# Kernel optimization log

Measured on AMD Instinct MI355X. Metric: run time of the kernel, lower is better.

The kernel has to match this reference:

```python
import jax, jax.numpy as jnp
import numpy as np

LOG2PI = float(np.log(2.0 * np.pi))
B, D = 8192, 4096


def setup_inputs() -> dict:
    key = jax.random.key(0)
    k1, k2, k3, k4, k5 = jax.random.split(key, 5)
    return {
        "z": jax.random.normal(k1, (B, D), dtype=jnp.float32),
        "mean": jax.random.normal(k2, (B, D), dtype=jnp.float32),
        "log_sd": jax.random.normal(k3, (B, D), dtype=jnp.float32),
        "target": jax.random.randint(k4, (B,), 0, 2, dtype=jnp.int64 if jax.config.jax_enable_x64 else jnp.int32),
        "logdet": jax.random.normal(k5, (B,), dtype=jnp.float32),
    }


def reference(z, mean, log_sd, target, logdet):
    # Per-class (binary) masked statistics, exactly matching the torch forward:
    #   mu_cls = mean[target==j].mean(0); log_sd_cls likewise;
    #   log_p  = gaussian_log_p(z_cls, mu_cls, log_sd_cls).sum(feature).mean(batch)
    def per_class(j):
        m = (target == j).astype(z.dtype)          # (B,)
        cnt = m.sum()
        ld_mean = (logdet * m).sum() / cnt          # scalar
        mu = (mean * m[:, None]).sum(0) / cnt       # (D,)
        lsd = (log_sd * m[:, None]).sum(0) / cnt    # (D,)
        # gaussian log-prob summed over features, per sample -> (B,)
        lp = (-0.5 * LOG2PI - lsd
              - 0.5 * (z - mu) ** 2 * jnp.exp(-2.0 * lsd)).sum(1)
        lp_mean = (lp * m).sum() / cnt              # masked mean over class members
        return ld_mean, mu, lsd, lp_mean

    res = [per_class(j) for j in (0, 1)]
    logdet_total = jnp.stack([r[0] for r in res])   # (2,)
    mus_per_class = jnp.stack([r[1] for r in res])  # (2, D)
    log_sds_per_class = jnp.stack([r[2] for r in res])  # (2, D)
    log_p_total = jnp.stack([r[3] for r in res])    # (2,)
    prior_logprob = (log_p_total + logdet_total).mean()
    return prior_logprob, mus_per_class, log_sds_per_class, log_p_total
```

## Files before the change

kernel.cpp:

```cpp
#include <hip/hip_runtime.h>

#define B_SZ 8192
#define D_SZ 4096
#define PC   128
#define RP   (B_SZ / PC)


__device__ __forceinline__ void acc4(float4& a, const float4 v) {
    a.x += v.x; a.y += v.y; a.z += v.z; a.w += v.w;
}
__device__ __forceinline__ void fma4(float4& a, const float4 v, const float k) {
    a.x = fmaf(v.x, k, a.x); a.y = fmaf(v.y, k, a.y);
    a.z = fmaf(v.z, k, a.z); a.w = fmaf(v.w, k, a.w);
}
__device__ __forceinline__ float4 sq4(const float4 v) {
    return {v.x * v.x, v.y * v.y, v.z * v.z, v.w * v.w};
}

__global__ __launch_bounds__(256, 4)
void colsum_kernel(const float* __restrict__ z,
                   const float* __restrict__ mean,
                   const float* __restrict__ lsd,
                   const int* __restrict__ target,
                   float* __restrict__ part) {
    const int col = blockIdx.x * 1024 + (threadIdx.x << 2);
    const int r   = blockIdx.y;
    const size_t base0 = (size_t)(r * RP) * D_SZ + col;

    const float* pz = z    + base0;
    const float* pm = mean + base0;
    const float* pl = lsd  + base0;
    const int*   pt = target + r * RP;

    float4 mA = {0,0,0,0}, m1 = {0,0,0,0};
    float4 lA = {0,0,0,0}, l1 = {0,0,0,0};
    float4 zA = {0,0,0,0}, z1 = {0,0,0,0};
    float4 qA = {0,0,0,0}, q1 = {0,0,0,0};

    for (int it = 0; it < RP / 4; ++it) {
        const float4 vz0 = *(const float4*)(pz);
        const float4 vz1 = *(const float4*)(pz + 1 * D_SZ);
        const float4 vz2 = *(const float4*)(pz + 2 * D_SZ);
        const float4 vz3 = *(const float4*)(pz + 3 * D_SZ);
        const float4 vm0 = *(const float4*)(pm);
        const float4 vm1 = *(const float4*)(pm + 1 * D_SZ);
        const float4 vm2 = *(const float4*)(pm + 2 * D_SZ);
        const float4 vm3 = *(const float4*)(pm + 3 * D_SZ);
        const float4 vl0 = *(const float4*)(pl);
        const float4 vl1 = *(const float4*)(pl + 1 * D_SZ);
        const float4 vl2 = *(const float4*)(pl + 2 * D_SZ);
        const float4 vl3 = *(const float4*)(pl + 3 * D_SZ);
        const int4   t   = *(const int4*)(pt);
        __builtin_amdgcn_sched_barrier(0);

        const float k0 = (t.x == 1) ? 1.f : 0.f;
        const float k1 = (t.y == 1) ? 1.f : 0.f;
        const float k2 = (t.z == 1) ? 1.f : 0.f;
        const float k3 = (t.w == 1) ? 1.f : 0.f;

        acc4(mA, vm0); fma4(m1, vm0, k0);
        acc4(mA, vm1); fma4(m1, vm1, k1);
        acc4(mA, vm2); fma4(m1, vm2, k2);
        acc4(mA, vm3); fma4(m1, vm3, k3);

        acc4(lA, vl0); fma4(l1, vl0, k0);
        acc4(lA, vl1); fma4(l1, vl1, k1);
        acc4(lA, vl2); fma4(l1, vl2, k2);
        acc4(lA, vl3); fma4(l1, vl3, k3);

        acc4(zA, vz0); fma4(z1, vz0, k0);
        acc4(zA, vz1); fma4(z1, vz1, k1);
        acc4(zA, vz2); fma4(z1, vz2, k2);
        acc4(zA, vz3); fma4(z1, vz3, k3);

        const float4 q0 = sq4(vz0); acc4(qA, q0); fma4(q1, q0, k0);
        const float4 qq1 = sq4(vz1); acc4(qA, qq1); fma4(q1, qq1, k1);
        const float4 q2 = sq4(vz2); acc4(qA, q2); fma4(q1, q2, k2);
        const float4 q3 = sq4(vz3); acc4(qA, q3); fma4(q1, q3, k3);

        pz += 4 * D_SZ; pm += 4 * D_SZ; pl += 4 * D_SZ; pt += 4;
    }

    *(float4*)(part + ((size_t)(0 * PC + r)) * D_SZ + col) = mA;
    *(float4*)(part + ((size_t)(1 * PC + r)) * D_SZ + col) = m1;
    *(float4*)(part + ((size_t)(2 * PC + r)) * D_SZ + col) = lA;
    *(float4*)(part + ((size_t)(3 * PC + r)) * D_SZ + col) = l1;
    *(float4*)(part + ((size_t)(4 * PC + r)) * D_SZ + col) = zA;
    *(float4*)(part + ((size_t)(5 * PC + r)) * D_SZ + col) = z1;
    *(float4*)(part + ((size_t)(6 * PC + r)) * D_SZ + col) = qA;
    *(float4*)(part + ((size_t)(7 * PC + r)) * D_SZ + col) = q1;
}

__global__ __launch_bounds__(256)
void reduce_count_kernel(const float* __restrict__ part,
                         const int* __restrict__ target,
                         const float* __restrict__ logdet,
                         float* __restrict__ red,
                         float* __restrict__ sc) {
    if (blockIdx.x == 64) {
        __shared__ float rsm[3][4];
        float c = 0.f, a = 0.f, o = 0.f;
#pragma unroll
        for (int k = 0; k < 8; ++k) {
            const int i = k * 1024 + (threadIdx.x << 2);
            const int4   t = *(const int4*)(target + i);
            const float4 l = *(const float4*)(logdet + i);
            const float n0 = (t.x == 1) ? 1.f : 0.f;
            const float n1 = (t.y == 1) ? 1.f : 0.f;
            const float n2 = (t.z == 1) ? 1.f : 0.f;
            const float n3 = (t.w == 1) ? 1.f : 0.f;
            c += n0 + n1 + n2 + n3;
            a += l.x + l.y + l.z + l.w;
            o += l.x * n0 + l.y * n1 + l.z * n2 + l.w * n3;
        }
        for (int off = 32; off > 0; off >>= 1) {
            c += __shfl_down(c, off);
            a += __shfl_down(a, off);
            o += __shfl_down(o, off);
        }
        const int w = threadIdx.x >> 6;
        if ((threadIdx.x & 63) == 0) { rsm[0][w] = c; rsm[1][w] = a; rsm[2][w] = o; }
        __syncthreads();
        if (threadIdx.x == 0) {
            sc[0] = rsm[0][0] + rsm[0][1] + rsm[0][2] + rsm[0][3];
            sc[1] = rsm[1][0] + rsm[1][1] + rsm[1][2] + rsm[1][3];
            sc[2] = rsm[2][0] + rsm[2][1] + rsm[2][2] + rsm[2][3];
        }
        return;
    }
    const int seg = blockIdx.x >> 3;
    const int sub = blockIdx.x & 7;
    const int col = (sub >> 1) * 1024 + (threadIdx.x << 2);
    const int r0  = (sub & 1) * (PC / 2);
    float4 acc = {0,0,0,0};
    for (int r = r0; r < r0 + PC / 2; ++r) {
        const float4 v = *(const float4*)(part + ((size_t)seg * PC + r) * D_SZ + col);
        acc4(acc, v);
    }
    *(float4*)(red + ((size_t)((sub & 1) * 8 + seg)) * D_SZ + col) = acc;
}

__global__ __launch_bounds__(256)
void finalize_cols_kernel(const float* __restrict__ red,
                          const float* __restrict__ sc,
                          double* __restrict__ dslots,
                          float* __restrict__ out) {
    const int d = blockIdx.x * 256 + threadIdx.x;
    const float cnt1 = sc[0];
    const float cnt0 = (float)B_SZ - cnt1;

#define RSEG(s) (red[(s) * D_SZ + d] + red[(8 + (s)) * D_SZ + d])
    const float ma = RSEG(0), m1 = RSEG(1);
    const float la = RSEG(2), l1 = RSEG(3);
    const float za = RSEG(4), z1 = RSEG(5);
    const float qa = RSEG(6), q1 = RSEG(7);
#undef RSEG

    const float mu1 = m1 / cnt1, mu0 = (ma - m1) / cnt0;
    const float ls1 = l1 / cnt1, ls0 = (la - l1) / cnt0;

    out[1 + d]            = mu0;
    out[1 + D_SZ + d]     = mu1;
    out[1 + 2 * D_SZ + d] = ls0;
    out[1 + 3 * D_SZ + d] = ls1;

    const float z0 = za - z1, q0 = qa - q1;
    const double w0 = 0.5 * exp(-2.0 * (double)ls0);
    const double w1 = 0.5 * exp(-2.0 * (double)ls1);
    double S0 = w0 * ((double)q0 - 2.0 * (double)mu0 * (double)z0 + (double)cnt0 * (double)mu0 * (double)mu0);
    double S1 = w1 * ((double)q1 - 2.0 * (double)mu1 * (double)z1 + (double)cnt1 * (double)mu1 * (double)mu1);
    double L0 = (double)ls0;
    double L1 = (double)ls1;

    for (int off = 32; off > 0; off >>= 1) {
        S0 += __shfl_down(S0, off);
        S1 += __shfl_down(S1, off);
        L0 += __shfl_down(L0, off);
        L1 += __shfl_down(L1, off);
    }
    if ((threadIdx.x & 63) == 0) {
        double* wd = dslots + (blockIdx.x * 4 + (threadIdx.x >> 6)) * 4;
        wd[0] = S0; wd[1] = S1; wd[2] = L0; wd[3] = L1;
    }
}

__global__ void finalize_scalars_kernel(const float* __restrict__ sc,
                                        const double* __restrict__ dslots,
                                        float* __restrict__ out) {
    const double* p = dslots + threadIdx.x * 4;
    double S0 = p[0], S1 = p[1], L0 = p[2], L1 = p[3];
    for (int off = 32; off > 0; off >>= 1) {
        S0 += __shfl_down(S0, off);
        S1 += __shfl_down(S1, off);
        L0 += __shfl_down(L0, off);
        L1 += __shfl_down(L1, off);
    }
    if (threadIdx.x == 0) {
        const double LOG2PI = 1.8378770664093453;
        const double cnt1 = (double)sc[0];
        const double cnt0 = (double)B_SZ - cnt1;
        const double ldm1 = (double)sc[2] / cnt1;
        const double ldm0 = ((double)sc[1] - (double)sc[2]) / cnt0;

        const double c0 = -0.5 * LOG2PI * (double)D_SZ - L0;
        const double c1 = -0.5 * LOG2PI * (double)D_SZ - L1;
        const double lp0 = c0 - S0 / cnt0;
        const double lp1 = c1 - S1 / cnt1;

        out[1 + 4 * D_SZ + 0] = (float)lp0;
        out[1 + 4 * D_SZ + 1] = (float)lp1;
        out[0] = (float)(0.5 * ((lp0 + ldm0) + (lp1 + ldm1)));
    }
}

extern "C" void kernel_launch(void* const* d_in, const int* in_sizes, int n_in,
                              void* d_out, int out_size, void* d_ws, size_t ws_size,
                              hipStream_t stream) {
    const float* z      = (const float*)d_in[0];
    const float* mean   = (const float*)d_in[1];
    const float* log_sd = (const float*)d_in[2];
    const int*   target = (const int*)d_in[3];
    const float* logdet = (const float*)d_in[4];
    float* out = (float*)d_out;
    float* ws  = (float*)d_ws;

    float*  part   = ws;
    float*  red    = ws + (size_t)PC * 8 * D_SZ;
    float*  sc     = red + 16 * D_SZ;
    double* dslots = (double*)(sc + 8);

    colsum_kernel<<<dim3(D_SZ / 1024, PC), 256, 0, stream>>>(z, mean, log_sd, target, part);
    reduce_count_kernel<<<65, 256, 0, stream>>>(part, target, logdet, red, sc);
    finalize_cols_kernel<<<D_SZ / 256, 256, 0, stream>>>(red, sc, dslots, out);
    finalize_scalars_kernel<<<1, 64, 0, stream>>>(sc, dslots, out);
}
```

Baseline: 88.51 us.

## Double row partitions, fold count reduction into stage1, widen partial reduce

```diff
diff --git a/kernel.cpp b/kernel.cpp
--- a/kernel.cpp
+++ b/kernel.cpp
@@ -2,8 +2,6 @@
 
 #define B_SZ 8192
 #define D_SZ 4096
-#define PC   128
-#define RP   (B_SZ / PC)
 
 
 __device__ __forceinline__ void acc4(float4& a, const float4 v) {
@@ -17,87 +15,18 @@
     return {v.x * v.x, v.y * v.y, v.z * v.z, v.w * v.w};
 }
 
+template <int PC>
 __global__ __launch_bounds__(256, 4)
-void colsum_kernel(const float* __restrict__ z,
+void stage1_kernel(const float* __restrict__ z,
                    const float* __restrict__ mean,
                    const float* __restrict__ lsd,
                    const int* __restrict__ target,
-                   float* __restrict__ part) {
-    const int col = blockIdx.x * 1024 + (threadIdx.x << 2);
-    const int r   = blockIdx.y;
-    const size_t base0 = (size_t)(r * RP) * D_SZ + col;
-
-    const float* pz = z    + base0;
-    const float* pm = mean + base0;
-    const float* pl = lsd  + base0;
-    const int*   pt = target + r * RP;
-
-    float4 mA = {0,0,0,0}, m1 = {0,0,0,0};
-    float4 lA = {0,0,0,0}, l1 = {0,0,0,0};
-    float4 zA = {0,0,0,0}, z1 = {0,0,0,0};
-    float4 qA = {0,0,0,0}, q1 = {0,0,0,0};
-
-    for (int it = 0; it < RP / 4; ++it) {
-        const float4 vz0 = *(const float4*)(pz);
-        const float4 vz1 = *(const float4*)(pz + 1 * D_SZ);
-        const float4 vz2 = *(const float4*)(pz + 2 * D_SZ);
-        const float4 vz3 = *(const float4*)(pz + 3 * D_SZ);
-        const float4 vm0 = *(const float4*)(pm);
-        const float4 vm1 = *(const float4*)(pm + 1 * D_SZ);
-        const float4 vm2 = *(const float4*)(pm + 2 * D_SZ);
-        const float4 vm3 = *(const float4*)(pm + 3 * D_SZ);
-        const float4 vl0 = *(const float4*)(pl);
-        const float4 vl1 = *(const float4*)(pl + 1 * D_SZ);
-        const float4 vl2 = *(const float4*)(pl + 2 * D_SZ);
-        const float4 vl3 = *(const float4*)(pl + 3 * D_SZ);
-        const int4   t   = *(const int4*)(pt);
-        __builtin_amdgcn_sched_barrier(0);
-
-        const float k0 = (t.x == 1) ? 1.f : 0.f;
-        const float k1 = (t.y == 1) ? 1.f : 0.f;
-        const float k2 = (t.z == 1) ? 1.f : 0.f;
-        const float k3 = (t.w == 1) ? 1.f : 0.f;
-
-        acc4(mA, vm0); fma4(m1, vm0, k0);
-        acc4(mA, vm1); fma4(m1, vm1, k1);
-        acc4(mA, vm2); fma4(m1, vm2, k2);
-        acc4(mA, vm3); fma4(m1, vm3, k3);
-
-        acc4(lA, vl0); fma4(l1, vl0, k0);
-        acc4(lA, vl1); fma4(l1, vl1, k1);
-        acc4(lA, vl2); fma4(l1, vl2, k2);
-        acc4(lA, vl3); fma4(l1, vl3, k3);
-
-        acc4(zA, vz0); fma4(z1, vz0, k0);
-        acc4(zA, vz1); fma4(z1, vz1, k1);
-        acc4(zA, vz2); fma4(z1, vz2, k2);
-        acc4(zA, vz3); fma4(z1, vz3, k3);
-
-        const float4 q0 = sq4(vz0); acc4(qA, q0); fma4(q1, q0, k0);
-        const float4 qq1 = sq4(vz1); acc4(qA, qq1); fma4(q1, qq1, k1);
-        const float4 q2 = sq4(vz2); acc4(qA, q2); fma4(q1, q2, k2);
-        const float4 q3 = sq4(vz3); acc4(qA, q3); fma4(q1, q3, k3);
-
-        pz += 4 * D_SZ; pm += 4 * D_SZ; pl += 4 * D_SZ; pt += 4;
-    }
-
-    *(float4*)(part + ((size_t)(0 * PC + r)) * D_SZ + col) = mA;
-    *(float4*)(part + ((size_t)(1 * PC + r)) * D_SZ + col) = m1;
-    *(float4*)(part + ((size_t)(2 * PC + r)) * D_SZ + col) = lA;
-    *(float4*)(part + ((size_t)(3 * PC + r)) * D_SZ + col) = l1;
-    *(float4*)(part + ((size_t)(4 * PC + r)) * D_SZ + col) = zA;
-    *(float4*)(part + ((size_t)(5 * PC + r)) * D_SZ + col) = z1;
-    *(float4*)(part + ((size_t)(6 * PC + r)) * D_SZ + col) = qA;
-    *(float4*)(part + ((size_t)(7 * PC + r)) * D_SZ + col) = q1;
-}
-
-__global__ __launch_bounds__(256)
-void reduce_count_kernel(const float* __restrict__ part,
-                         const int* __restrict__ target,
-                         const float* __restrict__ logdet,
-                         float* __restrict__ red,
-                         float* __restrict__ sc) {
-    if (blockIdx.x == 64) {
+                   const float* __restrict__ logdet,
+                   float* __restrict__ part,
+                   float* __restrict__ sc) {
+    constexpr int RP = B_SZ / PC;
+
+    if (blockIdx.x == 4 * PC) {
         __shared__ float rsm[3][4];
         float c = 0.f, a = 0.f, o = 0.f;
 #pragma unroll
@@ -128,16 +57,89 @@
         }
         return;
     }
-    const int seg = blockIdx.x >> 3;
-    const int sub = blockIdx.x & 7;
-    const int col = (sub >> 1) * 1024 + (threadIdx.x << 2);
-    const int r0  = (sub & 1) * (PC / 2);
+
+    const int col = (blockIdx.x & 3) * 1024 + (threadIdx.x << 2);
+    const int r   = blockIdx.x >> 2;
+    const size_t base0 = (size_t)(r * RP) * D_SZ + col;
+
+    const float* pz = z    + base0;
+    const float* pm = mean + base0;
+    const float* pl = lsd  + base0;
+    const int*   pt = target + r * RP;
+
+    float4 mA = {0,0,0,0}, m1 = {0,0,0,0};
+    float4 lA = {0,0,0,0}, l1 = {0,0,0,0};
+    float4 zA = {0,0,0,0}, z1 = {0,0,0,0};
+    float4 qA = {0,0,0,0}, q1 = {0,0,0,0};
+
+    for (int it = 0; it < RP / 4; ++it) {
+        const float4 vz0 = *(const float4*)(pz);
+        const float4 vz1 = *(const float4*)(pz + 1 * D_SZ);
+        const float4 vz2 = *(const float4*)(pz + 2 * D_SZ);
+        const float4 vz3 = *(const float4*)(pz + 3 * D_SZ);
+        const float4 vm0 = *(const float4*)(pm);
+        const float4 vm1 = *(const float4*)(pm + 1 * D_SZ);
+        const float4 vm2 = *(const float4*)(pm + 2 * D_SZ);
+        const float4 vm3 = *(const float4*)(pm + 3 * D_SZ);
+        const float4 vl0 = *(const float4*)(pl);
+        const float4 vl1 = *(const float4*)(pl + 1 * D_SZ);
+        const float4 vl2 = *(const float4*)(pl + 2 * D_SZ);
+        const float4 vl3 = *(const float4*)(pl + 3 * D_SZ);
+        const int4   t   = *(const int4*)(pt);
+        __builtin_amdgcn_sched_barrier(0);
+
+        const float k0 = (t.x == 1) ? 1.f : 0.f;
+        const float k1 = (t.y == 1) ? 1.f : 0.f;
+        const float k2 = (t.z == 1) ? 1.f : 0.f;
+        const float k3 = (t.w == 1) ? 1.f : 0.f;
+
+        acc4(mA, vm0); fma4(m1, vm0, k0);
+        acc4(mA, vm1); fma4(m1, vm1, k1);
+        acc4(mA, vm2); fma4(m1, vm2, k2);
+        acc4(mA, vm3); fma4(m1, vm3, k3);
+
+        acc4(lA, vl0); fma4(l1, vl0, k0);
+        acc4(lA, vl1); fma4(l1, vl1, k1);
+        acc4(lA, vl2); fma4(l1, vl2, k2);
+        acc4(lA, vl3); fma4(l1, vl3, k3);
+
+        acc4(zA, vz0); fma4(z1, vz0, k0);
+        acc4(zA, vz1); fma4(z1, vz1, k1);
+        acc4(zA, vz2); fma4(z1, vz2, k2);
+        acc4(zA, vz3); fma4(z1, vz3, k3);
+
+        const float4 q0  = sq4(vz0); acc4(qA, q0);  fma4(q1, q0,  k0);
+        const float4 qq1 = sq4(vz1); acc4(qA, qq1); fma4(q1, qq1, k1);
+        const float4 q2  = sq4(vz2); acc4(qA, q2);  fma4(q1, q2,  k2);
+        const float4 q3  = sq4(vz3); acc4(qA, q3);  fma4(q1, q3,  k3);
+
+        pz += 4 * D_SZ; pm += 4 * D_SZ; pl += 4 * D_SZ; pt += 4;
+    }
+
+    *(float4*)(part + ((size_t)(0 * PC + r)) * D_SZ + col) = mA;
+    *(float4*)(part + ((size_t)(1 * PC + r)) * D_SZ + col) = m1;
+    *(float4*)(part + ((size_t)(2 * PC + r)) * D_SZ + col) = lA;
+    *(float4*)(part + ((size_t)(3 * PC + r)) * D_SZ + col) = l1;
+    *(float4*)(part + ((size_t)(4 * PC + r)) * D_SZ + col) = zA;
+    *(float4*)(part + ((size_t)(5 * PC + r)) * D_SZ + col) = z1;
+    *(float4*)(part + ((size_t)(6 * PC + r)) * D_SZ + col) = qA;
+    *(float4*)(part + ((size_t)(7 * PC + r)) * D_SZ + col) = q1;
+}
+
+__global__ __launch_bounds__(256)
+void reduce_kernel(const float* __restrict__ part,
+                   float* __restrict__ red, int PC_) {
+    const int seg = blockIdx.x >> 4;
+    const int rem = blockIdx.x & 15;
+    const int col = (rem >> 2) * 1024 + (threadIdx.x << 2);
+    const int q   = rem & 3;
+    const int rq  = PC_ >> 2;
     float4 acc = {0,0,0,0};
-    for (int r = r0; r < r0 + PC / 2; ++r) {
-        const float4 v = *(const float4*)(part + ((size_t)seg * PC + r) * D_SZ + col);
+    for (int r = q * rq; r < (q + 1) * rq; ++r) {
+        const float4 v = *(const float4*)(part + ((size_t)seg * PC_ + r) * D_SZ + col);
         acc4(acc, v);
     }
-    *(float4*)(red + ((size_t)((sub & 1) * 8 + seg)) * D_SZ + col) = acc;
+    *(float4*)(red + ((size_t)(q * 8 + seg)) * D_SZ + col) = acc;
 }
 
 __global__ __launch_bounds__(256)
@@ -149,7 +151,8 @@
     const float cnt1 = sc[0];
     const float cnt0 = (float)B_SZ - cnt1;
 
-#define RSEG(s) (red[(s) * D_SZ + d] + red[(8 + (s)) * D_SZ + d])
+#define RSEG(s) (red[(0 * 8 + (s)) * D_SZ + d] + red[(1 * 8 + (s)) * D_SZ + d] + \
+                 red[(2 * 8 + (s)) * D_SZ + d] + red[(3 * 8 + (s)) * D_SZ + d])
     const float ma = RSEG(0), m1 = RSEG(1);
     const float la = RSEG(2), l1 = RSEG(3);
     const float za = RSEG(4), z1 = RSEG(5);
@@ -224,13 +227,20 @@
     float* out = (float*)d_out;
     float* ws  = (float*)d_ws;
 
+    const size_t need256 = ((size_t)256 * 8 * D_SZ + 32 * D_SZ + 8) * 4 + 64 * 4 * 8;
+    const int PC = (ws_size >= need256) ? 256 : 128;
+
     float*  part   = ws;
     float*  red    = ws + (size_t)PC * 8 * D_SZ;
-    float*  sc     = red + 16 * D_SZ;
+    float*  sc     = red + 32 * D_SZ;
     double* dslots = (double*)(sc + 8);
 
-    colsum_kernel<<<dim3(D_SZ / 1024, PC), 256, 0, stream>>>(z, mean, log_sd, target, part);
-    reduce_count_kernel<<<65, 256, 0, stream>>>(part, target, logdet, red, sc);
+    if (PC == 256) {
+        stage1_kernel<256><<<4 * 256 + 1, 256, 0, stream>>>(z, mean, log_sd, target, logdet, part, sc);
+    } else {
+        stage1_kernel<128><<<4 * 128 + 1, 256, 0, stream>>>(z, mean, log_sd, target, logdet, part, sc);
+    }
+    reduce_kernel<<<128, 256, 0, stream>>>(part, red, PC);
     finalize_cols_kernel<<<D_SZ / 256, 256, 0, stream>>>(red, sc, dslots, out);
     finalize_scalars_kernel<<<1, 64, 0, stream>>>(sc, dslots, out);
 }
```

Measured after the change: 108.1 us. 1.22x slower.
